# Performance work log

Measured on AMD Instinct MI355X. Metric: run time of the kernel, lower is better.

## Reference

```python
import jax, jax.numpy as jnp
import numpy as np

GYRO_COV = 0.00016968 ** 2
ACC_COV = 0.002 ** 2
GRAVITY = 9.81007


def _skew(v):
    # v: (..., 3) -> (..., 3, 3)
    x, y, z = v[..., 0], v[..., 1], v[..., 2]
    O = jnp.zeros_like(x)
    return jnp.stack([
        jnp.stack([O, -z, y], -1),
        jnp.stack([z, O, -x], -1),
        jnp.stack([-y, x, O], -1)], -2)


def _exp_and_jr(w):
    """SO3 Exp map (rotation matrix) and right Jacobian of w = omega*dt. w: (B,3)."""
    t2 = jnp.sum(w * w, axis=-1)[..., None, None]          # (B,1,1)
    small = t2 < 1e-8
    t2s = jnp.where(small, 1.0, t2)                        # safe denominators
    t = jnp.sqrt(t2s)
    A = jnp.where(small, 1.0 - t2 / 6.0, jnp.sin(t) / t)           # sin(t)/t
    Bc = jnp.where(small, 0.5 - t2 / 24.0, (1.0 - jnp.cos(t)) / t2s)  # (1-cos)/t^2
    C = jnp.where(small, 1.0 / 6.0 - t2 / 120.0, (t - jnp.sin(t)) / (t2s * t))  # (t-sin)/t^3
    K = _skew(w)
    K2 = K @ K
    I = jnp.eye(3, dtype=w.dtype)
    R = I + A * K + Bc * K2
    Jr = I - Bc * K + C * K2
    return R, Jr


def _preintegrate(dt, gyro, acc, init_pos, init_rot, init_vel):
    B, F = dt.shape[0], dt.shape[1]
    dtype = dt.dtype
    I3 = jnp.eye(3, dtype=dtype)

    def step(carry, xs):
        Dr, Dv, Dp, cov, t = carry
        dtk, wk, ak = xs                      # (B,1), (B,3), (B,3)
        dR, Jr = _exp_and_jr(wk * dtk)        # (B,3,3) each
        Ra = jnp.einsum('bij,bj->bi', Dr, ak) # Delta_R_ik @ a_k
        Dp_n = Dp + Dv * dtk + 0.5 * Ra * dtk ** 2
        Dv_n = Dv + Ra * dtk
        Dr_n = Dr @ dR
        # --- 9x9 covariance propagation ---
        dt_ = dtk[..., None]                  # (B,1,1)
        Ha = (Dr @ _skew(ak))                 # Delta_R_ik @ skew(a_k)
        Ib = jnp.broadcast_to(I3, Ha.shape)
        Z = jnp.zeros_like(Ha)
        A = jnp.concatenate([
            jnp.concatenate([jnp.swapaxes(dR, -1, -2), Z, Z], -1),
            jnp.concatenate([-Ha * dt_, Ib, Z], -1),
            jnp.concatenate([-0.5 * Ha * dt_ ** 2, Ib * dt_, Ib], -1)], -2)  # (B,9,9)
        Bg = Jr * dt_                                                        # (B,3,3)
        Ba = jnp.concatenate([Dr * dt_, 0.5 * Dr * dt_ ** 2], -2)           # (B,6,3)
        Ng = GYRO_COV * (Bg @ jnp.swapaxes(Bg, -1, -2))
        Na = ACC_COV * (Ba @ jnp.swapaxes(Ba, -1, -2))
        N = jnp.zeros_like(cov).at[:, :3, :3].set(Ng).at[:, 3:, 3:].set(Na)
        cov_n = A @ cov @ jnp.swapaxes(A, -1, -2) + N
        t_n = t + dtk
        return (Dr_n, Dv_n, Dp_n, cov_n, t_n), (Dr_n, Dv_n, Dp_n, t_n)

    carry0 = (jnp.broadcast_to(I3, (B, 3, 3)),
              jnp.zeros((B, 3), dtype),
              jnp.zeros((B, 3), dtype),
              jnp.zeros((B, 9, 9), dtype),
              jnp.zeros((B, 1), dtype))
    xs = (jnp.moveaxis(dt, 1, 0), jnp.moveaxis(gyro, 1, 0), jnp.moveaxis(acc, 1, 0))
    (Dr, Dv, Dp, cov, t), (Drs, Dvs, Dps, ts) = jax.lax.scan(step, carry0, xs)
    Drs = jnp.moveaxis(Drs, 0, 1)   # (B,F,3,3)
    Dvs = jnp.moveaxis(Dvs, 0, 1)   # (B,F,3)
    Dps = jnp.moveaxis(Dps, 0, 1)   # (B,F,3)
    ts = jnp.moveaxis(ts, 0, 1)     # (B,F,1)
    grav = jnp.array([0.0, 0.0, GRAVITY], dtype=dtype)
    rot = jnp.einsum('ij,bfjk->bfik', init_rot, Drs)                       # R_j = R_i * dR_ij
    vel = init_vel + jnp.einsum('ij,bfj->bfi', init_rot, Dvs) - grav * ts
    pos = (init_pos + init_vel * ts
           + jnp.einsum('ij,bfj->bfi', init_rot, Dps) - 0.5 * grav * ts ** 2)
    return rot, vel, pos, cov


def setup_inputs() -> dict:
    key = jax.random.key(0)
    k1, k2, k3 = jax.random.split(key, 3)
    B, F = 512, 2048
    dt = 0.004 * jax.random.uniform(k1, (B, F, 1), dtype=jnp.float32) + 0.001  # ~200-1000Hz
    gyro = 0.5 * jax.random.normal(k2, (B, F, 3), dtype=jnp.float32)
    acc = 2.0 * jax.random.normal(k3, (B, F, 3), dtype=jnp.float32)
    return {"dt": dt, "gyro": gyro, "acc": acc,
            "init_pos": jnp.zeros(3, jnp.float32),
            "init_rot": jnp.eye(3, dtype=jnp.float32),
            "init_vel": jnp.zeros(3, jnp.float32)}


def reference(dt, gyro, acc, init_pos, init_rot, init_vel):
    return _preintegrate(dt, gyro, acc, init_pos, init_rot, init_vel)
```

## Files before the change

### kernel.cpp

```cpp
#include <hip/hip_runtime.h>
#include <cstddef>

#define FCNT 2048
#define SEG 512
#define LSTEP 4

#define GRAV 9.81007f
#define GYRO_COV (0.00016968f * 0.00016968f)
#define ACC_COV (0.002f * 0.002f)

__device__ __forceinline__ void exp_coefs(float t2, float& A, float& Bc, float& Cc) {
  A  = 1.f     + t2 * (-1.f/6.f   + t2 * (1.f/120.f  + t2 * (-1.f/5040.f)));
  Bc = 0.5f    + t2 * (-1.f/24.f  + t2 * (1.f/720.f  + t2 * (-1.f/40320.f)));
  Cc = 1.f/6.f + t2 * (-1.f/120.f + t2 * (1.f/5040.f + t2 * (-1.f/362880.f)));
  if (t2 > 0.004f) {
    float t = sqrtf(t2);
    float sn = __sinf(t), cs = __cosf(t);
    A  = sn / t;
    Bc = (1.f - cs) / t2;
    Cc = (t - sn) / (t2 * t);
  }
}

__device__ __forceinline__ void make_dR(float w0, float w1, float w2, float t2,
                                        float A, float Bc, float* dR) {
  float w01 = w0*w1, w02 = w0*w2, w12 = w1*w2;
  dR[0] = 1.f + Bc*(w0*w0 - t2); dR[1] = Bc*w01 - A*w2;         dR[2] = Bc*w02 + A*w1;
  dR[3] = Bc*w01 + A*w2;         dR[4] = 1.f + Bc*(w1*w1 - t2); dR[5] = Bc*w12 - A*w0;
  dR[6] = Bc*w02 - A*w1;         dR[7] = Bc*w12 + A*w0;         dR[8] = 1.f + Bc*(w2*w2 - t2);
}

__device__ __forceinline__ void mm3(const float* a, const float* b, float* c) {
#pragma unroll
  for (int i = 0; i < 3; ++i) {
    float a0 = a[i*3+0], a1 = a[i*3+1], a2 = a[i*3+2];
    c[i*3+0] = a0*b[0] + a1*b[3] + a2*b[6];
    c[i*3+1] = a0*b[1] + a1*b[4] + a2*b[7];
    c[i*3+2] = a0*b[2] + a1*b[5] + a2*b[8];
  }
}

__device__ __forceinline__ void conjT(const float* R, const float* Mp, float* M) {
  float tmp[9];
#pragma unroll
  for (int i = 0; i < 3; ++i)
#pragma unroll
    for (int j = 0; j < 3; ++j)
      tmp[i*3+j] = R[0+i]*Mp[0+j] + R[3+i]*Mp[3+j] + R[6+i]*Mp[6+j];
  mm3(tmp, R, M);
}

__device__ __forceinline__ void compose16(const float* pa, const float* stv, float* o) {
  float nR[9];
  mm3(pa, stv, nR);
  float nv0 = pa[9]  + pa[0]*stv[9] + pa[1]*stv[10] + pa[2]*stv[11];
  float nv1 = pa[10] + pa[3]*stv[9] + pa[4]*stv[10] + pa[5]*stv[11];
  float nv2 = pa[11] + pa[6]*stv[9] + pa[7]*stv[10] + pa[8]*stv[11];
  float qt = stv[15];
  float np0 = pa[12] + pa[9]*qt  + pa[0]*stv[12] + pa[1]*stv[13] + pa[2]*stv[14];
  float np1 = pa[13] + pa[10]*qt + pa[3]*stv[12] + pa[4]*stv[13] + pa[5]*stv[14];
  float np2 = pa[14] + pa[11]*qt + pa[6]*stv[12] + pa[7]*stv[13] + pa[8]*stv[14];
  float nt = pa[15] + qt;
#pragma unroll
  for (int i = 0; i < 9; ++i) o[i] = nR[i];
  o[9]=nv0; o[10]=nv1; o[11]=nv2;
  o[12]=np0; o[13]=np1; o[14]=np2;
  o[15]=nt;
}

__device__ __forceinline__ void set_identity16(float* o) {
  o[0]=1;o[1]=0;o[2]=0; o[3]=0;o[4]=1;o[5]=0; o[6]=0;o[7]=0;o[8]=1;
#pragma unroll
  for (int i = 9; i < 16; ++i) o[i] = 0.f;
}

__device__ __forceinline__ void load_seg(const float* __restrict__ dtp,
                                         const float* __restrict__ gyp,
                                         const float* __restrict__ acp,
                                         size_t base, float* dl, float* gl, float* al) {
  const float4 x0 = *reinterpret_cast<const float4*>(dtp + base);
  dl[0]=x0.x; dl[1]=x0.y; dl[2]=x0.z; dl[3]=x0.w;
  const float4* qg = reinterpret_cast<const float4*>(gyp + base*3);
  const float4* qa = reinterpret_cast<const float4*>(acp + base*3);
#pragma unroll
  for (int i = 0; i < 3; ++i) {
    float4 xg = qg[i];
    gl[i*4+0]=xg.x; gl[i*4+1]=xg.y; gl[i*4+2]=xg.z; gl[i*4+3]=xg.w;
    float4 xa = qa[i];
    al[i*4+0]=xa.x; al[i*4+1]=xa.y; al[i*4+2]=xa.z; al[i*4+3]=xa.w;
  }
}

__device__ __forceinline__ void integrate_seg(const float* dl, const float* gl,
                                              const float* al, float* st) {
  set_identity16(st);
#pragma unroll
  for (int j = 0; j < LSTEP; ++j) {
    float dd = dl[j];
    float w0 = gl[j*3+0]*dd, w1 = gl[j*3+1]*dd, w2 = gl[j*3+2]*dd;
    float t2 = w0*w0 + w1*w1 + w2*w2;
    float A, Bc, Cc;
    exp_coefs(t2, A, Bc, Cc);
    (void)Cc;
    float dR[9];
    make_dR(w0, w1, w2, t2, A, Bc, dR);
    float a0 = al[j*3+0], a1 = al[j*3+1], a2 = al[j*3+2];
    float Ra0 = st[0]*a0 + st[1]*a1 + st[2]*a2;
    float Ra1 = st[3]*a0 + st[4]*a1 + st[5]*a2;
    float Ra2 = st[6]*a0 + st[7]*a1 + st[8]*a2;
    float hh = 0.5f*dd*dd;
    st[12] += st[9]*dd  + hh*Ra0;
    st[13] += st[10]*dd + hh*Ra1;
    st[14] += st[11]*dd + hh*Ra2;
    st[9] += Ra0*dd; st[10] += Ra1*dd; st[11] += Ra2*dd;
    float Rn[9];
    mm3(st, dR, Rn);
#pragma unroll
    for (int i = 0; i < 9; ++i) st[i] = Rn[i];
    st[15] += dd;
  }
}

__global__ __launch_bounds__(SEG, 2)
void imu_fused(const float* __restrict__ dtp, const float* __restrict__ gyp,
               const float* __restrict__ acp, const float* __restrict__ ip0,
               const float* __restrict__ iR0, const float* __restrict__ iv0,
               float* __restrict__ out, int B)
{
  __shared__ float rstage[FCNT*9];
  __shared__ float wtot[16*8];
  __shared__ float rbuf[8][48];
  __shared__ float tsum[48];

  const int s = threadIdx.x;
  const int lane = s & 63;
  const int wid = s >> 6;
  const int b = blockIdx.x;
  const size_t base = (size_t)b*FCNT + (size_t)s*LSTEP;
  const size_t NBF = (size_t)B*FCNT;
  float* orot = out;
  float* ovel = out + NBF*9;
  float* opos = out + NBF*12;
  float* ocov = out + NBF*15;

  float st[16];
  {
    float dl[LSTEP], gl[LSTEP*3], al[LSTEP*3];
    load_seg(dtp, gyp, acp, base, dl, gl, al);
    integrate_seg(dl, gl, al, st);
  }

#pragma unroll
  for (int off = 1; off < 64; off <<= 1) {
    float pa[16];
#pragma unroll
    for (int i = 0; i < 16; ++i) pa[i] = __shfl_up(st[i], off);
    if (lane >= off) compose16(pa, st, st);
  }
  if (lane == 63) {
#pragma unroll
    for (int i = 0; i < 16; ++i) wtot[i*8 + wid] = st[i];
  }
  __syncthreads();
  if (s < 8) {
    float t[16];
#pragma unroll
    for (int i = 0; i < 16; ++i) t[i] = wtot[i*8 + s];
#pragma unroll
    for (int off = 1; off < 8; off <<= 1) {
      float pa[16];
#pragma unroll
      for (int i = 0; i < 16; ++i) pa[i] = __shfl_up(t[i], off);
      if (s >= off) compose16(pa, t, t);
    }
#pragma unroll
    for (int i = 0; i < 16; ++i) wtot[i*8 + s] = t[i];
  }
  __syncthreads();

  float TF[16];
#pragma unroll
  for (int i = 0; i < 16; ++i) TF[i] = wtot[i*8 + 7];

  float cr[16];
  {
    float lex[16];
#pragma unroll
    for (int i = 0; i < 16; ++i) lex[i] = __shfl_up(st[i], 1);
    if (lane == 0) set_identity16(lex);
    if (wid == 0) {
#pragma unroll
      for (int i = 0; i < 16; ++i) cr[i] = lex[i];
    } else {
      float wx[16];
#pragma unroll
      for (int i = 0; i < 16; ++i) wx[i] = wtot[i*8 + wid - 1];
      compose16(wx, lex, cr);
    }
  }

  float R0g[9];
#pragma unroll
  for (int i = 0; i < 9; ++i) R0g[i] = iR0[i];
  const float p0x = ip0[0], p0y = ip0[1], p0z = ip0[2];
  const float v0x = iv0[0], v0y = iv0[1], v0z = iv0[2];

  const float Tt = TF[15];
  const float Tvp0 = R0g[0]*TF[9] + R0g[1]*TF[10] + R0g[2]*TF[11];
  const float Tvp1 = R0g[3]*TF[9] + R0g[4]*TF[10] + R0g[5]*TF[11];
  const float Tvp2 = R0g[6]*TF[9] + R0g[7]*TF[10] + R0g[8]*TF[11];
  const float Tpp0 = R0g[0]*TF[12] + R0g[1]*TF[13] + R0g[2]*TF[14];
  const float Tpp1 = R0g[3]*TF[12] + R0g[4]*TF[13] + R0g[5]*TF[14];
  const float Tpp2 = R0g[6]*TF[12] + R0g[7]*TF[13] + R0g[8]*TF[14];

  float tR[9];
  mm3(R0g, cr, tR);
  float tv0 = R0g[0]*cr[9] + R0g[1]*cr[10] + R0g[2]*cr[11];
  float tv1 = R0g[3]*cr[9] + R0g[4]*cr[10] + R0g[5]*cr[11];
  float tv2 = R0g[6]*cr[9] + R0g[7]*cr[10] + R0g[8]*cr[11];
  float tp0 = R0g[0]*cr[12] + R0g[1]*cr[13] + R0g[2]*cr[14];
  float tp1 = R0g[3]*cr[12] + R0g[4]*cr[13] + R0g[5]*cr[14];
  float tp2 = R0g[6]*cr[12] + R0g[7]*cr[13] + R0g[8]*cr[14];
  float ctt = cr[15];

  float dl[LSTEP], gl[LSTEP*3], al[LSTEP*3];
  load_seg(dtp, gyp, acp, base, dl, gl, al);

  float aS0=0,aS1=0,aS2=0,aS3=0,aS4=0,aS5=0;
  float aU0=0,aU1=0,aU2=0,aU3=0,aU4=0,aU5=0,aU6=0,aU7=0,aU8=0;
  float aV0=0,aV1=0,aV2=0,aV3=0,aV4=0,aV5=0,aV6=0,aV7=0,aV8=0;
  float b220=0,b221=0,b222=0,b223=0,b224=0,b225=0;
  float b230=0,b231=0,b232=0,b233=0,b234=0,b235=0,b236=0,b237=0,b238=0;
  float b330=0,b331=0,b332=0,b333=0,b334=0,b335=0;
  float sa=0.f, sb=0.f, sc=0.f;
  float vloc[LSTEP*3], ploc[LSTEP*3];

#pragma unroll
  for (int j = 0; j < LSTEP; ++j) {
    const float dd = dl[j];
    const float w0 = gl[j*3+0]*dd, w1 = gl[j*3+1]*dd, w2 = gl[j*3+2]*dd;
    const float t2 = w0*w0 + w1*w1 + w2*w2;
    float A, Bc, Cc;
    exp_coefs(t2, A, Bc, Cc);
    float dR[9];
    make_dR(w0, w1, w2, t2, A, Bc, dR);
    const float a0 = al[j*3+0], a1 = al[j*3+1], a2 = al[j*3+2];
    const float Ra0 = tR[0]*a0 + tR[1]*a1 + tR[2]*a2;
    const float Ra1 = tR[3]*a0 + tR[4]*a1 + tR[5]*a2;
    const float Ra2 = tR[6]*a0 + tR[7]*a1 + tR[8]*a2;
    const float hh = 0.5f*dd*dd;
    tp0 += tv0*dd + hh*Ra0;
    tp1 += tv1*dd + hh*Ra1;
    tp2 += tv2*dd + hh*Ra2;
    tv0 += Ra0*dd; tv1 += Ra1*dd; tv2 += Ra2*dd;
    float Rn[9];
    mm3(tR, dR, Rn);
#pragma unroll
    for (int i = 0; i < 9; ++i) {
      tR[i] = Rn[i];
      rstage[((size_t)s*LSTEP + j)*9 + i] = Rn[i];
    }
    ctt += dd;
    vloc[j*3+0] = v0x + tv0;
    vloc[j*3+1] = v0y + tv1;
    vloc[j*3+2] = v0z + tv2 - GRAV*ctt;
    ploc[j*3+0] = p0x + v0x*ctt + tp0;
    ploc[j*3+1] = p0y + v0y*ctt + tp1;
    ploc[j*3+2] = p0z + v0z*ctt + tp2 - 0.5f*GRAV*ctt*ctt;

    const float sg  = GYRO_COV*dd*dd;
    const float eps = 2.f*Cc - Bc*Bc - Cc*Cc*t2;
    const float alpha = sg*(1.f - eps*t2);
    const float beta  = sg*eps;
    const float u0 = tR[0]*w0 + tR[1]*w1 + tR[2]*w2;
    const float u1 = tR[3]*w0 + tR[4]*w1 + tR[5]*w2;
    const float u2 = tR[6]*w0 + tR[7]*w1 + tR[8]*w2;
    const float z = Tt - ctt;
    const float wv0 = Tvp0 - tv0, wv1 = Tvp1 - tv1, wv2 = Tvp2 - tv2;
    const float wp0 = Tpp0 - tp0 - z*tv0;
    const float wp1 = Tpp1 - tp1 - z*tv1;
    const float wp2 = Tpp2 - tp2 - z*tv2;
    const float c0 = wv1*u2 - wv2*u1;
    const float c1 = wv2*u0 - wv0*u2;
    const float c2 = wv0*u1 - wv1*u0;
    const float d0 = wp1*u2 - wp2*u1;
    const float d1 = wp2*u0 - wp0*u2;
    const float d2 = wp0*u1 - wp1*u0;
    const float bu0 = beta*u0, bu1 = beta*u1, bu2 = beta*u2;
    const float bc0 = beta*c0, bc1 = beta*c1, bc2 = beta*c2;
    const float bd0 = beta*d0, bd1 = beta*d1, bd2 = beta*d2;
    const float av0 = alpha*wv0, av1 = alpha*wv1, av2 = alpha*wv2;
    const float ap0 = alpha*wp0, ap1 = alpha*wp1, ap2 = alpha*wp2;
    const float nv2_ = wv0*wv0 + wv1*wv1 + wv2*wv2;
    const float np2_ = wp0*wp0 + wp1*wp1 + wp2*wp2;
    const float dvp  = wv0*wp0 + wv1*wp1 + wv2*wp2;
    aS0 += alpha + bu0*u0; aS1 += bu0*u1; aS2 += bu0*u2;
    aS3 += alpha + bu1*u1; aS4 += bu1*u2; aS5 += alpha + bu2*u2;
    aU0 += -bu0*c0;        aU1 += -av2 - bu0*c1;  aU2 +=  av1 - bu0*c2;
    aU3 +=  av2 - bu1*c0;  aU4 += -bu1*c1;        aU5 += -av0 - bu1*c2;
    aU6 += -av1 - bu2*c0;  aU7 +=  av0 - bu2*c1;  aU8 += -bu2*c2;
    aV0 += -bu0*d0;        aV1 += -ap2 - bu0*d1;  aV2 +=  ap1 - bu0*d2;
    aV3 +=  ap2 - bu1*d0;  aV4 += -bu1*d1;        aV5 += -ap0 - bu1*d2;
    aV6 += -ap1 - bu2*d0;  aV7 +=  ap0 - bu2*d1;  aV8 += -bu2*d2;
    b220 += av0*wv0 - alpha*nv2_ - bc0*c0;
    b221 += av0*wv1 - bc0*c1;
    b222 += av0*wv2 - bc0*c2;
    b223 += av1*wv1 - alpha*nv2_ - bc1*c1;
    b224 += av1*wv2 - bc1*c2;
    b225 += av2*wv2 - alpha*nv2_ - bc2*c2;
    b230 += ap0*wv0 - alpha*dvp - bc0*d0;
    b231 += ap0*wv1 - bc0*d1;
    b232 += ap0*wv2 - bc0*d2;
    b233 += ap1*wv0 - bc1*d0;
    b234 += ap1*wv1 - alpha*dvp - bc1*d1;
    b235 += ap1*wv2 - bc1*d2;
    b236 += ap2*wv0 - bc2*d0;
    b237 += ap2*wv1 - bc2*d1;
    b238 += ap2*wv2 - alpha*dvp - bc2*d2;
    b330 += ap0*wp0 - alpha*np2_ - bd0*d0;
    b331 += ap0*wp1 - bd0*d1;
    b332 += ap0*wp2 - bd0*d2;
    b333 += ap1*wp1 - alpha*np2_ - bd1*d1;
    b334 += ap1*wp2 - bd1*d2;
    b335 += ap2*wp2 - alpha*np2_ - bd2*d2;
    const float dsq = dd*dd;
    const float aa = ACC_COV*dsq;
    const float bbq = 0.5f*ACC_COV*dsq*dd;
    sa += aa;
    sb += aa*z + bbq;
    sc += z*(aa*z + 2.f*bbq) + 0.25f*ACC_COV*dsq*dsq;
  }
  __syncthreads();

  {
    const float4* sm4 = reinterpret_cast<const float4*>(rstage);
    float4* g4 = reinterpret_cast<float4*>(orot + (size_t)b * FCNT * 9);
#pragma unroll
    for (int k = 0; k < 9; ++k)
      g4[k*SEG + s] = sm4[k*SEG + s];
  }
  {
    float4* vq = reinterpret_cast<float4*>(ovel + base*3);
#pragma unroll
    for (int k = 0; k < LSTEP*3/4; ++k)
      vq[k] = make_float4(vloc[k*4+0], vloc[k*4+1], vloc[k*4+2], vloc[k*4+3]);
    float4* pq = reinterpret_cast<float4*>(opos + base*3);
#pragma unroll
    for (int k = 0; k < LSTEP*3/4; ++k)
      pq[k] = make_float4(ploc[k*4+0], ploc[k*4+1], ploc[k*4+2], ploc[k*4+3]);
  }

  {
    float red[48] = {aS0,aS1,aS2,aS3,aS4,aS5,
                     aU0,aU1,aU2,aU3,aU4,aU5,aU6,aU7,aU8,
                     aV0,aV1,aV2,aV3,aV4,aV5,aV6,aV7,aV8,
                     b220,b221,b222,b223,b224,b225,
                     b230,b231,b232,b233,b234,b235,b236,b237,b238,
                     b330,b331,b332,b333,b334,b335,
                     sa,sb,sc};
#pragma unroll
    for (int i = 0; i < 48; ++i) {
      float x = red[i];
      x += __shfl_down(x, 32);
      x += __shfl_down(x, 16);
      x += __shfl_down(x, 8);
      x += __shfl_down(x, 4);
      x += __shfl_down(x, 2);
      x += __shfl_down(x, 1);
      red[i] = x;
    }
    if (lane == 0) {
#pragma unroll
      for (int i = 0; i < 48; ++i) rbuf[wid][i] = red[i];
    }
  }
  __syncthreads();
  if (s < 48) {
    float acc = rbuf[0][s];
#pragma unroll
    for (int w = 1; w < 8; ++w) acc += rbuf[w][s];
    tsum[s] = acc;
  }
  __syncthreads();

  if (s == 0) {
    float T[48];
#pragma unroll
    for (int i = 0; i < 48; ++i) T[i] = tsum[i];
    float TR[9];
#pragma unroll
    for (int i = 0; i < 9; ++i) TR[i] = TF[i];
    float Rt[9] = {TR[0],TR[3],TR[6], TR[1],TR[4],TR[7], TR[2],TR[5],TR[8]};
    float Smp[9] = {T[0],T[1],T[2], T[1],T[3],T[4], T[2],T[4],T[5]};
    float Ump[9] = {T[6],T[7],T[8], T[9],T[10],T[11], T[12],T[13],T[14]};
    float Vmp[9] = {T[15],T[16],T[17], T[18],T[19],T[20], T[21],T[22],T[23]};
    float W22p[9]= {T[24],T[25],T[26], T[25],T[27],T[28], T[26],T[28],T[29]};
    float W23p[9]= {T[30],T[31],T[32], T[33],T[34],T[35], T[36],T[37],T[38]};
    float W33p[9]= {T[39],T[40],T[41], T[40],T[42],T[43], T[41],T[43],T[44]};
    float Sm[9], Um[9], Vm[9], W22[9], W23[9], W33[9];
    conjT(R0g, Smp, Sm);
    conjT(R0g, Ump, Um);
    conjT(R0g, Vmp, Vm);
    conjT(R0g, W22p, W22);
    conjT(R0g, W23p, W23);
    conjT(R0g, W33p, W33);
    const float ssa = T[45], ssb = T[46], ssc = T[47];
    float T1[9], C11[9], C12[9], C13[9];
    mm3(Rt, Sm, T1);
    mm3(T1, TR, C11);
    mm3(Rt, Um, C12);
    mm3(Rt, Vm, C13);
    float* co = ocov + (size_t)b * 81;
#pragma unroll
    for (int i = 0; i < 3; ++i) {
#pragma unroll
      for (int jj = 0; jj < 3; ++jj) {
        co[i*9 + jj]       = C11[i*3+jj];
        co[i*9 + 3 + jj]   = C12[i*3+jj];
        co[i*9 + 6 + jj]   = C13[i*3+jj];
        co[(3+i)*9 + jj]     = C12[jj*3+i];
        co[(3+i)*9 + 3 + jj] = -W22[i*3+jj] + (i==jj ? ssa : 0.f);
        co[(3+i)*9 + 6 + jj] = -W23[i*3+jj] + (i==jj ? ssb : 0.f);
        co[(6+i)*9 + jj]     = C13[jj*3+i];
        co[(6+i)*9 + 3 + jj] = -W23[jj*3+i] + (i==jj ? ssb : 0.f);
        co[(6+i)*9 + 6 + jj] = -W33[i*3+jj] + (i==jj ? ssc : 0.f);
      }
    }
  }
}

extern "C" void kernel_launch(void* const* d_in, const int* in_sizes, int n_in,
                              void* d_out, int out_size, void* d_ws, size_t ws_size,
                              hipStream_t stream) {
  const float* dt   = (const float*)d_in[0];
  const float* gyro = (const float*)d_in[1];
  const float* acc  = (const float*)d_in[2];
  const float* ip   = (const float*)d_in[3];
  const float* iR   = (const float*)d_in[4];
  const float* iv   = (const float*)d_in[5];
  float* out = (float*)d_out;
  const int B = in_sizes[0] / FCNT;
  imu_fused<<<dim3(B), dim3(SEG), 0, stream>>>(dt, gyro, acc, ip, iR, iv, out, B);
}
```

Measured before the change: 51.08 us.

## Split per-block sequence into two halves to halve rotation staging LDS

After: 58.29 us. +14.1%, slower.

```diff
diff --git a/kernel.cpp b/kernel.cpp
--- a/kernel.cpp
+++ b/kernel.cpp
@@ -3,7 +3,8 @@
 
 #define FCNT 2048
 #define SEG 512
-#define LSTEP 4
+#define LSTEP 2
+#define HALFF 1024
 
 #define GRAV 9.81007f
 #define GYRO_COV (0.00016968f * 0.00016968f)
@@ -74,25 +75,33 @@
   for (int i = 9; i < 16; ++i) o[i] = 0.f;
 }
 
-__device__ __forceinline__ void load_seg(const float* __restrict__ dtp,
-                                         const float* __restrict__ gyp,
-                                         const float* __restrict__ acp,
-                                         size_t base, float* dl, float* gl, float* al) {
-  const float4 x0 = *reinterpret_cast<const float4*>(dtp + base);
-  dl[0]=x0.x; dl[1]=x0.y; dl[2]=x0.z; dl[3]=x0.w;
-  const float4* qg = reinterpret_cast<const float4*>(gyp + base*3);
-  const float4* qa = reinterpret_cast<const float4*>(acp + base*3);
+__device__ __forceinline__ float uf(float x) {
+  return __uint_as_float(__builtin_amdgcn_readfirstlane(__float_as_uint(x)));
+}
+
+__device__ __forceinline__ void lds_barrier() {
+  asm volatile("s_waitcnt lgkmcnt(0)" ::: "memory");
+  __builtin_amdgcn_s_barrier();
+  asm volatile("" ::: "memory");
+}
+
+__device__ __forceinline__ void load_seg2(const float* __restrict__ dtp,
+                                          const float* __restrict__ gyp,
+                                          const float* __restrict__ acp,
+                                          size_t base, float* dl, float* gl, float* al) {
+  const float2 x0 = *reinterpret_cast<const float2*>(dtp + base);
+  dl[0]=x0.x; dl[1]=x0.y;
+  const float2* qg = reinterpret_cast<const float2*>(gyp + base*3);
+  const float2* qa = reinterpret_cast<const float2*>(acp + base*3);
 #pragma unroll
   for (int i = 0; i < 3; ++i) {
-    float4 xg = qg[i];
-    gl[i*4+0]=xg.x; gl[i*4+1]=xg.y; gl[i*4+2]=xg.z; gl[i*4+3]=xg.w;
-    float4 xa = qa[i];
-    al[i*4+0]=xa.x; al[i*4+1]=xa.y; al[i*4+2]=xa.z; al[i*4+3]=xa.w;
-  }
-}
-
-__device__ __forceinline__ void integrate_seg(const float* dl, const float* gl,
-                                              const float* al, float* st) {
+    float2 xg = qg[i]; gl[i*2+0]=xg.x; gl[i*2+1]=xg.y;
+    float2 xa = qa[i]; al[i*2+0]=xa.x; al[i*2+1]=xa.y;
+  }
+}
+
+__device__ __forceinline__ void integrate2(const float* dl, const float* gl,
+                                           const float* al, float* st) {
   set_identity16(st);
 #pragma unroll
   for (int j = 0; j < LSTEP; ++j) {
@@ -121,14 +130,63 @@
   }
 }
 
+__device__ __forceinline__ void scan_half(float* st, float* wt, int s, int lane, int wid) {
+#pragma unroll
+  for (int off = 1; off < 64; off <<= 1) {
+    float pa[16];
+#pragma unroll
+    for (int i = 0; i < 16; ++i) pa[i] = __shfl_up(st[i], off);
+    if (lane >= off) compose16(pa, st, st);
+  }
+  if (lane == 63) {
+#pragma unroll
+    for (int i = 0; i < 16; ++i) wt[i*8 + wid] = st[i];
+  }
+  __syncthreads();
+  if (s < 8) {
+    float t[16];
+#pragma unroll
+    for (int i = 0; i < 16; ++i) t[i] = wt[i*8 + s];
+#pragma unroll
+    for (int off = 1; off < 8; off <<= 1) {
+      float pa[16];
+#pragma unroll
+      for (int i = 0; i < 16; ++i) pa[i] = __shfl_up(t[i], off);
+      if (s >= off) compose16(pa, t, t);
+    }
+#pragma unroll
+    for (int i = 0; i < 16; ++i) wt[i*8 + s] = t[i];
+  }
+  __syncthreads();
+}
+
+__device__ __forceinline__ void excl_carry(const float* st, const float* wt, float* cr,
+                                           int lane, int wid) {
+  float lex[16];
+#pragma unroll
+  for (int i = 0; i < 16; ++i) lex[i] = __shfl_up(st[i], 1);
+  if (lane == 0) set_identity16(lex);
+  if (wid == 0) {
+#pragma unroll
+    for (int i = 0; i < 16; ++i) cr[i] = lex[i];
+  } else {
+    float wx[16];
+#pragma unroll
+    for (int i = 0; i < 16; ++i) wx[i] = wt[i*8 + wid - 1];
+    compose16(wx, lex, cr);
+  }
+}
+
 __global__ __launch_bounds__(SEG, 2)
 void imu_fused(const float* __restrict__ dtp, const float* __restrict__ gyp,
                const float* __restrict__ acp, const float* __restrict__ ip0,
                const float* __restrict__ iR0, const float* __restrict__ iv0,
                float* __restrict__ out, int B)
 {
-  __shared__ float rstage[FCNT*9];
-  __shared__ float wtot[16*8];
+  __shared__ float rstage[HALFF*9];
+  __shared__ float park[16][SEG];
+  __shared__ float wtot0[16*8];
+  __shared__ float wtot1[16*8];
   __shared__ float rbuf[8][48];
   __shared__ float tsum[48];
 
@@ -136,67 +194,39 @@
   const int lane = s & 63;
   const int wid = s >> 6;
   const int b = blockIdx.x;
-  const size_t base = (size_t)b*FCNT + (size_t)s*LSTEP;
   const size_t NBF = (size_t)B*FCNT;
   float* orot = out;
   float* ovel = out + NBF*9;
   float* opos = out + NBF*12;
   float* ocov = out + NBF*15;
 
-  float st[16];
-  {
-    float dl[LSTEP], gl[LSTEP*3], al[LSTEP*3];
-    load_seg(dtp, gyp, acp, base, dl, gl, al);
-    integrate_seg(dl, gl, al, st);
-  }
-
-#pragma unroll
-  for (int off = 1; off < 64; off <<= 1) {
-    float pa[16];
-#pragma unroll
-    for (int i = 0; i < 16; ++i) pa[i] = __shfl_up(st[i], off);
-    if (lane >= off) compose16(pa, st, st);
-  }
-  if (lane == 63) {
-#pragma unroll
-    for (int i = 0; i < 16; ++i) wtot[i*8 + wid] = st[i];
-  }
-  __syncthreads();
-  if (s < 8) {
-    float t[16];
-#pragma unroll
-    for (int i = 0; i < 16; ++i) t[i] = wtot[i*8 + s];
-#pragma unroll
-    for (int off = 1; off < 8; off <<= 1) {
-      float pa[16];
-#pragma unroll
-      for (int i = 0; i < 16; ++i) pa[i] = __shfl_up(t[i], off);
-      if (s >= off) compose16(pa, t, t);
-    }
-#pragma unroll
-    for (int i = 0; i < 16; ++i) wtot[i*8 + s] = t[i];
-  }
-  __syncthreads();
-
-  float TF[16];
-#pragma unroll
-  for (int i = 0; i < 16; ++i) TF[i] = wtot[i*8 + 7];
-
-  float cr[16];
-  {
-    float lex[16];
-#pragma unroll
-    for (int i = 0; i < 16; ++i) lex[i] = __shfl_up(st[i], 1);
-    if (lane == 0) set_identity16(lex);
-    if (wid == 0) {
-#pragma unroll
-      for (int i = 0; i < 16; ++i) cr[i] = lex[i];
-    } else {
-      float wx[16];
-#pragma unroll
-      for (int i = 0; i < 16; ++i) wx[i] = wtot[i*8 + wid - 1];
-      compose16(wx, lex, cr);
-    }
+  const size_t base0 = (size_t)b*FCNT + (size_t)s*LSTEP;
+  const size_t base1 = base0 + HALFF;
+
+  float dl0[LSTEP], gl0[LSTEP*3], al0[LSTEP*3];
+  load_seg2(dtp, gyp, acp, base0, dl0, gl0, al0);
+  float cr0[16];
+  {
+    float st[16];
+    integrate2(dl0, gl0, al0, st);
+    scan_half(st, wtot0, s, lane, wid);
+    excl_carry(st, wtot0, cr0, lane, wid);
+  }
+
+  {
+    float dl1[LSTEP], gl1[LSTEP*3], al1[LSTEP*3];
+    load_seg2(dtp, gyp, acp, base1, dl1, gl1, al1);
+    float st[16];
+    integrate2(dl1, gl1, al1, st);
+    scan_half(st, wtot1, s, lane, wid);
+    float cr1[16];
+    excl_carry(st, wtot1, cr1, lane, wid);
+    float T0[16];
+#pragma unroll
+    for (int i = 0; i < 16; ++i) T0[i] = wtot0[i*8 + 7];
+    compose16(T0, cr1, cr1);
+#pragma unroll
+    for (int i = 0; i < 16; ++i) park[i][s] = cr1[i];
   }
 
   float R0g[9];
@@ -205,26 +235,20 @@
   const float p0x = ip0[0], p0y = ip0[1], p0z = ip0[2];
   const float v0x = iv0[0], v0y = iv0[1], v0z = iv0[2];
 
-  const float Tt = TF[15];
-  const float Tvp0 = R0g[0]*TF[9] + R0g[1]*TF[10] + R0g[2]*TF[11];
-  const float Tvp1 = R0g[3]*TF[9] + R0g[4]*TF[10] + R0g[5]*TF[11];
-  const float Tvp2 = R0g[6]*TF[9] + R0g[7]*TF[10] + R0g[8]*TF[11];
-  const float Tpp0 = R0g[0]*TF[12] + R0g[1]*TF[13] + R0g[2]*TF[14];
-  const float Tpp1 = R0g[3]*TF[12] + R0g[4]*TF[13] + R0g[5]*TF[14];
-  const float Tpp2 = R0g[6]*TF[12] + R0g[7]*TF[13] + R0g[8]*TF[14];
-
-  float tR[9];
-  mm3(R0g, cr, tR);
-  float tv0 = R0g[0]*cr[9] + R0g[1]*cr[10] + R0g[2]*cr[11];
-  float tv1 = R0g[3]*cr[9] + R0g[4]*cr[10] + R0g[5]*cr[11];
-  float tv2 = R0g[6]*cr[9] + R0g[7]*cr[10] + R0g[8]*cr[11];
-  float tp0 = R0g[0]*cr[12] + R0g[1]*cr[13] + R0g[2]*cr[14];
-  float tp1 = R0g[3]*cr[12] + R0g[4]*cr[13] + R0g[5]*cr[14];
-  float tp2 = R0g[6]*cr[12] + R0g[7]*cr[13] + R0g[8]*cr[14];
-  float ctt = cr[15];
-
-  float dl[LSTEP], gl[LSTEP*3], al[LSTEP*3];
-  load_seg(dtp, gyp, acp, base, dl, gl, al);
+  float Tt, Tvp0, Tvp1, Tvp2, Tpp0, Tpp1, Tpp2;
+  {
+    float T0[16], T1[16], TF[16];
+#pragma unroll
+    for (int i = 0; i < 16; ++i) { T0[i] = wtot0[i*8+7]; T1[i] = wtot1[i*8+7]; }
+    compose16(T0, T1, TF);
+    Tt   = uf(TF[15]);
+    Tvp0 = uf(R0g[0]*TF[9] + R0g[1]*TF[10] + R0g[2]*TF[11]);
+    Tvp1 = uf(R0g[3]*TF[9] + R0g[4]*TF[10] + R0g[5]*TF[11]);
+    Tvp2 = uf(R0g[6]*TF[9] + R0g[7]*TF[10] + R0g[8]*TF[11]);
+    Tpp0 = uf(R0g[0]*TF[12] + R0g[1]*TF[13] + R0g[2]*TF[14]);
+    Tpp1 = uf(R0g[3]*TF[12] + R0g[4]*TF[13] + R0g[5]*TF[14]);
+    Tpp2 = uf(R0g[6]*TF[12] + R0g[7]*TF[13] + R0g[8]*TF[14]);
+  }
 
   float aS0=0,aS1=0,aS2=0,aS3=0,aS4=0,aS5=0;
   float aU0=0,aU1=0,aU2=0,aU3=0,aU4=0,aU5=0,aU6=0,aU7=0,aU8=0;
@@ -233,121 +257,164 @@
   float b230=0,b231=0,b232=0,b233=0,b234=0,b235=0,b236=0,b237=0,b238=0;
   float b330=0,b331=0,b332=0,b333=0,b334=0,b335=0;
   float sa=0.f, sb=0.f, sc=0.f;
-  float vloc[LSTEP*3], ploc[LSTEP*3];
-
-#pragma unroll
-  for (int j = 0; j < LSTEP; ++j) {
-    const float dd = dl[j];
-    const float w0 = gl[j*3+0]*dd, w1 = gl[j*3+1]*dd, w2 = gl[j*3+2]*dd;
-    const float t2 = w0*w0 + w1*w1 + w2*w2;
-    float A, Bc, Cc;
-    exp_coefs(t2, A, Bc, Cc);
-    float dR[9];
-    make_dR(w0, w1, w2, t2, A, Bc, dR);
-    const float a0 = al[j*3+0], a1 = al[j*3+1], a2 = al[j*3+2];
-    const float Ra0 = tR[0]*a0 + tR[1]*a1 + tR[2]*a2;
-    const float Ra1 = tR[3]*a0 + tR[4]*a1 + tR[5]*a2;
-    const float Ra2 = tR[6]*a0 + tR[7]*a1 + tR[8]*a2;
-    const float hh = 0.5f*dd*dd;
-    tp0 += tv0*dd + hh*Ra0;
-    tp1 += tv1*dd + hh*Ra1;
-    tp2 += tv2*dd + hh*Ra2;
-    tv0 += Ra0*dd; tv1 += Ra1*dd; tv2 += Ra2*dd;
-    float Rn[9];
-    mm3(tR, dR, Rn);
-#pragma unroll
-    for (int i = 0; i < 9; ++i) {
-      tR[i] = Rn[i];
-      rstage[((size_t)s*LSTEP + j)*9 + i] = Rn[i];
+
+  auto merged_half = [&](int h, const float* dl, const float* gl, const float* al,
+                         float* tR, float tv0, float tv1, float tv2,
+                         float tp0, float tp1, float tp2, float ctt) {
+    float vloc[6], ploc[6];
+#pragma unroll
+    for (int j = 0; j < LSTEP; ++j) {
+      const float dd = dl[j];
+      const float w0 = gl[j*3+0]*dd, w1 = gl[j*3+1]*dd, w2 = gl[j*3+2]*dd;
+      const float t2 = w0*w0 + w1*w1 + w2*w2;
+      float A, Bc, Cc;
+      exp_coefs(t2, A, Bc, Cc);
+      float dR[9];
+      make_dR(w0, w1, w2, t2, A, Bc, dR);
+      const float a0 = al[j*3+0], a1 = al[j*3+1], a2 = al[j*3+2];
+      const float Ra0 = tR[0]*a0 + tR[1]*a1 + tR[2]*a2;
+      const float Ra1 = tR[3]*a0 + tR[4]*a1 + tR[5]*a2;
+      const float Ra2 = tR[6]*a0 + tR[7]*a1 + tR[8]*a2;
+      const float hh = 0.5f*dd*dd;
+      tp0 += tv0*dd + hh*Ra0;
+      tp1 += tv1*dd + hh*Ra1;
+      tp2 += tv2*dd + hh*Ra2;
+      tv0 += Ra0*dd; tv1 += Ra1*dd; tv2 += Ra2*dd;
+      float Rn[9];
+      mm3(tR, dR, Rn);
+#pragma unroll
+      for (int i = 0; i < 9; ++i) {
+        tR[i] = Rn[i];
+        rstage[(2*s + j)*9 + i] = Rn[i];
+      }
+      ctt += dd;
+      vloc[j*3+0] = v0x + tv0;
+      vloc[j*3+1] = v0y + tv1;
+      vloc[j*3+2] = v0z + tv2 - GRAV*ctt;
+      ploc[j*3+0] = p0x + v0x*ctt + tp0;
+      ploc[j*3+1] = p0y + v0y*ctt + tp1;
+      ploc[j*3+2] = p0z + v0z*ctt + tp2 - 0.5f*GRAV*ctt*ctt;
+
+      const float sg  = GYRO_COV*dd*dd;
+      const float eps = 2.f*Cc - Bc*Bc - Cc*Cc*t2;
+      const float alpha = sg*(1.f - eps*t2);
+      const float beta  = sg*eps;
+      const float u0 = tR[0]*w0 + tR[1]*w1 + tR[2]*w2;
+      const float u1 = tR[3]*w0 + tR[4]*w1 + tR[5]*w2;
+      const float u2 = tR[6]*w0 + tR[7]*w1 + tR[8]*w2;
+      const float z = Tt - ctt;
+      const float wv0 = Tvp0 - tv0, wv1 = Tvp1 - tv1, wv2 = Tvp2 - tv2;
+      const float wp0 = Tpp0 - tp0 - z*tv0;
+      const float wp1 = Tpp1 - tp1 - z*tv1;
+      const float wp2 = Tpp2 - tp2 - z*tv2;
+      const float c0 = wv1*u2 - wv2*u1;
+      const float c1 = wv2*u0 - wv0*u2;
+      const float c2 = wv0*u1 - wv1*u0;
+      const float d0 = wp1*u2 - wp2*u1;
+      const float d1 = wp2*u0 - wp0*u2;
+      const float d2 = wp0*u1 - wp1*u0;
+      const float bu0 = beta*u0, bu1 = beta*u1, bu2 = beta*u2;
+      const float bc0 = beta*c0, bc1 = beta*c1, bc2 = beta*c2;
+      const float bd0 = beta*d0, bd1 = beta*d1, bd2 = beta*d2;
+      const float av0 = alpha*wv0, av1 = alpha*wv1, av2 = alpha*wv2;
+      const float ap0 = alpha*wp0, ap1 = alpha*wp1, ap2 = alpha*wp2;
+      const float nv2_ = wv0*wv0 + wv1*wv1 + wv2*wv2;
+      const float np2_ = wp0*wp0 + wp1*wp1 + wp2*wp2;
+      const float dvp  = wv0*wp0 + wv1*wp1 + wv2*wp2;
+      aS0 += alpha + bu0*u0; aS1 += bu0*u1; aS2 += bu0*u2;
+      aS3 += alpha + bu1*u1; aS4 += bu1*u2; aS5 += alpha + bu2*u2;
+      aU0 += -bu0*c0;        aU1 += -av2 - bu0*c1;  aU2 +=  av1 - bu0*c2;
+      aU3 +=  av2 - bu1*c0;  aU4 += -bu1*c1;        aU5 += -av0 - bu1*c2;
+      aU6 += -av1 - bu2*c0;  aU7 +=  av0 - bu2*c1;  aU8 += -bu2*c2;
+      aV0 += -bu0*d0;        aV1 += -ap2 - bu0*d1;  aV2 +=  ap1 - bu0*d2;
+      aV3 +=  ap2 - bu1*d0;  aV4 += -bu1*d1;        aV5 += -ap0 - bu1*d2;
+      aV6 += -ap1 - bu2*d0;  aV7 +=  ap0 - bu2*d1;  aV8 += -bu2*d2;
+      b220 += av0*wv0 - alpha*nv2_ - bc0*c0;
+      b221 += av0*wv1 - bc0*c1;
+      b222 += av0*wv2 - bc0*c2;
+      b223 += av1*wv1 - alpha*nv2_ - bc1*c1;
+      b224 += av1*wv2 - bc1*c2;
+      b225 += av2*wv2 - alpha*nv2_ - bc2*c2;
+      b230 += ap0*wv0 - alpha*dvp - bc0*d0;
+      b231 += ap0*wv1 - bc0*d1;
+      b232 += ap0*wv2 - bc0*d2;
+      b233 += ap1*wv0 - bc1*d0;
+      b234 += ap1*wv1 - alpha*dvp - bc1*d1;
+      b235 += ap1*wv2 - bc1*d2;
+      b236 += ap2*wv0 - bc2*d0;
+      b237 += ap2*wv1 - bc2*d1;
+      b238 += ap2*wv2 - alpha*dvp - bc2*d2;
+      b330 += ap0*wp0 - alpha*np2_ - bd0*d0;
+      b331 += ap0*wp1 - bd0*d1;
+      b332 += ap0*wp2 - bd0*d2;
+      b333 += ap1*wp1 - alpha*np2_ - bd1*d1;
+      b334 += ap1*wp2 - bd1*d2;
+      b335 += ap2*wp2 - alpha*np2_ - bd2*d2;
+      const float dsq = dd*dd;
+      const float aa = ACC_COV*dsq;
+      const float bbq = 0.5f*ACC_COV*dsq*dd;
+      sa += aa;
+      sb += aa*z + bbq;
+      sc += z*(aa*z + 2.f*bbq) + 0.25f*ACC_COV*dsq*dsq;
     }
-    ctt += dd;
-    vloc[j*3+0] = v0x + tv0;
-    vloc[j*3+1] = v0y + tv1;
-    vloc[j*3+2] = v0z + tv2 - GRAV*ctt;
-    ploc[j*3+0] = p0x + v0x*ctt + tp0;
-    ploc[j*3+1] = p0y + v0y*ctt + tp1;
-    ploc[j*3+2] = p0z + v0z*ctt + tp2 - 0.5f*GRAV*ctt*ctt;
-
-    const float sg  = GYRO_COV*dd*dd;
-    const float eps = 2.f*Cc - Bc*Bc - Cc*Cc*t2;
-    const float alpha = sg*(1.f - eps*t2);
-    const float beta  = sg*eps;
-    const float u0 = tR[0]*w0 + tR[1]*w1 + tR[2]*w2;
-    const float u1 = tR[3]*w0 + tR[4]*w1 + tR[5]*w2;
-    const float u2 = tR[6]*w0 + tR[7]*w1 + tR[8]*w2;
-    const float z = Tt - ctt;
-    const float wv0 = Tvp0 - tv0, wv1 = Tvp1 - tv1, wv2 = Tvp2 - tv2;
-    const float wp0 = Tpp0 - tp0 - z*tv0;
-    const float wp1 = Tpp1 - tp1 - z*tv1;
-    const float wp2 = Tpp2 - tp2 - z*tv2;
-    const float c0 = wv1*u2 - wv2*u1;
-    const float c1 = wv2*u0 - wv0*u2;
-    const float c2 = wv0*u1 - wv1*u0;
-    const float d0 = wp1*u2 - wp2*u1;
-    const float d1 = wp2*u0 - wp0*u2;
-    const float d2 = wp0*u1 - wp1*u0;
-    const float bu0 = beta*u0, bu1 = beta*u1, bu2 = beta*u2;
-    const float bc0 = beta*c0, bc1 = beta*c1, bc2 = beta*c2;
-    const float bd0 = beta*d0, bd1 = beta*d1, bd2 = beta*d2;
-    const float av0 = alpha*wv0, av1 = alpha*wv1, av2 = alpha*wv2;
-    const float ap0 = alpha*wp0, ap1 = alpha*wp1, ap2 = alpha*wp2;
-    const float nv2_ = wv0*wv0 + wv1*wv1 + wv2*wv2;
-    const float np2_ = wp0*wp0 + wp1*wp1 + wp2*wp2;
-    const float dvp  = wv0*wp0 + wv1*wp1 + wv2*wp2;
-    aS0 += alpha + bu0*u0; aS1 += bu0*u1; aS2 += bu0*u2;
-    aS3 += alpha + bu1*u1; aS4 += bu1*u2; aS5 += alpha + bu2*u2;
-    aU0 += -bu0*c0;        aU1 += -av2 - bu0*c1;  aU2 +=  av1 - bu0*c2;
-    aU3 +=  av2 - bu1*c0;  aU4 += -bu1*c1;        aU5 += -av0 - bu1*c2;
-    aU6 += -av1 - bu2*c0;  aU7 +=  av0 - bu2*c1;  aU8 += -bu2*c2;
-    aV0 += -bu0*d0;        aV1 += -ap2 - bu0*d1;  aV2 +=  ap1 - bu0*d2;
-    aV3 +=  ap2 - bu1*d0;  aV4 += -bu1*d1;        aV5 += -ap0 - bu1*d2;
-    aV6 += -ap1 - bu2*d0;  aV7 +=  ap0 - bu2*d1;  aV8 += -bu2*d2;
-    b220 += av0*wv0 - alpha*nv2_ - bc0*c0;
-    b221 += av0*wv1 - bc0*c1;
-    b222 += av0*wv2 - bc0*c2;
-    b223 += av1*wv1 - alpha*nv2_ - bc1*c1;
-    b224 += av1*wv2 - bc1*c2;
-    b225 += av2*wv2 - alpha*nv2_ - bc2*c2;
-    b230 += ap0*wv0 - alpha*dvp - bc0*d0;
-    b231 += ap0*wv1 - bc0*d1;
-    b232 += ap0*wv2 - bc0*d2;
-    b233 += ap1*wv0 - bc1*d0;
-    b234 += ap1*wv1 - alpha*dvp - bc1*d1;
-    b235 += ap1*wv2 - bc1*d2;
-    b236 += ap2*wv0 - bc2*d0;
-    b237 += ap2*wv1 - bc2*d1;
-    b238 += ap2*wv2 - alpha*dvp - bc2*d2;
-    b330 += ap0*wp0 - alpha*np2_ - bd0*d0;
-    b331 += ap0*wp1 - bd0*d1;
-    b332 += ap0*wp2 - bd0*d2;
-    b333 += ap1*wp1 - alpha*np2_ - bd1*d1;
-    b334 += ap1*wp2 - bd1*d2;
-    b335 += ap2*wp2 - alpha*np2_ - bd2*d2;
-    const float dsq = dd*dd;
-    const float aa = ACC_COV*dsq;
-    const float bbq = 0.5f*ACC_COV*dsq*dd;
-    sa += aa;
-    sb += aa*z + bbq;
-    sc += z*(aa*z + 2.f*bbq) + 0.25f*ACC_COV*dsq*dsq;
-  }
-  __syncthreads();
-
-  {
-    const float4* sm4 = reinterpret_cast<const float4*>(rstage);
-    float4* g4 = reinterpret_cast<float4*>(orot + (size_t)b * FCNT * 9);
-#pragma unroll
-    for (int k = 0; k < 9; ++k)
-      g4[k*SEG + s] = sm4[k*SEG + s];
-  }
-  {
-    float4* vq = reinterpret_cast<float4*>(ovel + base*3);
-#pragma unroll
-    for (int k = 0; k < LSTEP*3/4; ++k)
-      vq[k] = make_float4(vloc[k*4+0], vloc[k*4+1], vloc[k*4+2], vloc[k*4+3]);
-    float4* pq = reinterpret_cast<float4*>(opos + base*3);
-#pragma unroll
-    for (int k = 0; k < LSTEP*3/4; ++k)
-      pq[k] = make_float4(ploc[k*4+0], ploc[k*4+1], ploc[k*4+2], ploc[k*4+3]);
+    const size_t vb = ((size_t)b*FCNT + (size_t)h*HALFF + 2*(size_t)s)*3;
+    float2* vq = reinterpret_cast<float2*>(ovel + vb);
+    vq[0] = make_float2(vloc[0], vloc[1]);
+    vq[1] = make_float2(vloc[2], vloc[3]);
+    vq[2] = make_float2(vloc[4], vloc[5]);
+    float2* pq = reinterpret_cast<float2*>(opos + vb);
+    pq[0] = make_float2(ploc[0], ploc[1]);
+    pq[1] = make_float2(ploc[2], ploc[3]);
+    pq[2] = make_float2(ploc[4], ploc[5]);
+  };
+
+  {
+    float tR[9];
+    mm3(R0g, cr0, tR);
+    float tv0 = R0g[0]*cr0[9] + R0g[1]*cr0[10] + R0g[2]*cr0[11];
+    float tv1 = R0g[3]*cr0[9] + R0g[4]*cr0[10] + R0g[5]*cr0[11];
+    float tv2 = R0g[6]*cr0[9] + R0g[7]*cr0[10] + R0g[8]*cr0[11];
+    float tp0 = R0g[0]*cr0[12] + R0g[1]*cr0[13] + R0g[2]*cr0[14];
+    float tp1 = R0g[3]*cr0[12] + R0g[4]*cr0[13] + R0g[5]*cr0[14];
+    float tp2 = R0g[6]*cr0[12] + R0g[7]*cr0[13] + R0g[8]*cr0[14];
+    merged_half(0, dl0, gl0, al0, tR, tv0, tv1, tv2, tp0, tp1, tp2, cr0[15]);
+  }
+
+  lds_barrier();
+
+  float dl1[LSTEP], gl1[LSTEP*3], al1[LSTEP*3];
+  load_seg2(dtp, gyp, acp, base1, dl1, gl1, al1);
+  {
+    const size_t go = ((size_t)b*FCNT)*9;
+#pragma unroll
+    for (int k = 0; k < 18; ++k)
+      orot[go + (size_t)k*SEG + s] = rstage[k*SEG + s];
+  }
+
+  lds_barrier();
+
+  {
+    float cr1[16];
+#pragma unroll
+    for (int i = 0; i < 16; ++i) cr1[i] = park[i][s];
+    float tR[9];
+    mm3(R0g, cr1, tR);
+    float tv0 = R0g[0]*cr1[9] + R0g[1]*cr1[10] + R0g[2]*cr1[11];
+    float tv1 = R0g[3]*cr1[9] + R0g[4]*cr1[10] + R0g[5]*cr1[11];
+    float tv2 = R0g[6]*cr1[9] + R0g[7]*cr1[10] + R0g[8]*cr1[11];
+    float tp0 = R0g[0]*cr1[12] + R0g[1]*cr1[13] + R0g[2]*cr1[14];
+    float tp1 = R0g[3]*cr1[12] + R0g[4]*cr1[13] + R0g[5]*cr1[14];
+    float tp2 = R0g[6]*cr1[12] + R0g[7]*cr1[13] + R0g[8]*cr1[14];
+    merged_half(1, dl1, gl1, al1, tR, tv0, tv1, tv2, tp0, tp1, tp2, cr1[15]);
+  }
+
+  lds_barrier();
+
+  {
+    const size_t go = ((size_t)b*FCNT + HALFF)*9;
+#pragma unroll
+    for (int k = 0; k < 18; ++k)
+      orot[go + (size_t)k*SEG + s] = rstage[k*SEG + s];
   }
 
   {
@@ -374,19 +441,23 @@
       for (int i = 0; i < 48; ++i) rbuf[wid][i] = red[i];
     }
   }
-  __syncthreads();
+  lds_barrier();
   if (s < 48) {
     float acc = rbuf[0][s];
 #pragma unroll
     for (int w = 1; w < 8; ++w) acc += rbuf[w][s];
     tsum[s] = acc;
   }
-  __syncthreads();
+  lds_barrier();
 
   if (s == 0) {
     float T[48];
 #pragma unroll
     for (int i = 0; i < 48; ++i) T[i] = tsum[i];
+    float T0[16], T1[16], TF[16];
+#pragma unroll
+    for (int i = 0; i < 16; ++i) { T0[i] = wtot0[i*8+7]; T1[i] = wtot1[i*8+7]; }
+    compose16(T0, T1, TF);
     float TR[9];
 #pragma unroll
     for (int i = 0; i < 9; ++i) TR[i] = TF[i];
@@ -405,9 +476,9 @@
     conjT(R0g, W23p, W23);
     conjT(R0g, W33p, W33);
     const float ssa = T[45], ssb = T[46], ssc = T[47];
-    float T1[9], C11[9], C12[9], C13[9];
-    mm3(Rt, Sm, T1);
-    mm3(T1, TR, C11);
+    float T1m[9], C11[9], C12[9], C13[9];
+    mm3(Rt, Sm, T1m);
+    mm3(T1m, TR, C11);
     mm3(Rt, Um, C12);
     mm3(Rt, Vm, C13);
     float* co = ocov + (size_t)b * 81;
```
